# Optimization experiments

Hardware: AMD Instinct MI355X
Metric: run time of the kernel (lower is better)

The kernel has to match this reference:

```python
import jax, jax.numpy as jnp
import numpy as np

H = 16      # num_heads
D = 1024    # hidden_dim
HD = D // H # head_dim = 64


def setup_inputs() -> dict:
    key = jax.random.key(0)
    ks = jax.random.split(key, 9)
    s = 1.0 / np.sqrt(D)
    return {
        "hidden_states": jax.random.normal(ks[0], (2, 2048, D), dtype=jnp.float32),
        "wq": jax.random.uniform(ks[1], (D, D), jnp.float32, -s, s),
        "bq": jax.random.uniform(ks[2], (D,), jnp.float32, -s, s),
        "wk": jax.random.uniform(ks[3], (D, D), jnp.float32, -s, s),
        "bk": jax.random.uniform(ks[4], (D,), jnp.float32, -s, s),
        "wv": jax.random.uniform(ks[5], (D, D), jnp.float32, -s, s),
        "bv": jax.random.uniform(ks[6], (D,), jnp.float32, -s, s),
        "wo": jax.random.uniform(ks[7], (D, D), jnp.float32, -s, s),
        "bo": jax.random.uniform(ks[8], (D,), jnp.float32, -s, s),
    }


def reference(hidden_states, wq, bq, wk, bk, wv, bv, wo, bo):
    B, L, _ = hidden_states.shape
    scale = HD ** -0.5
    # projections: [B,L,D] -> [B,H,L,HD]
    def split_heads(x):
        return x.reshape(B, L, H, HD).transpose(0, 2, 1, 3)
    q = split_heads(hidden_states @ wq.T + bq)
    k = split_heads(hidden_states @ wk.T + bk)
    v = split_heads(hidden_states @ wv.T + bv)
    # explicit [B,H,L,L] scores + softmax + weighted sum (faithful to source)
    scores = jnp.einsum("bhqd,bhkd->bhqk", q, k) * scale
    attn = jax.nn.softmax(scores, axis=-1)
    out = jnp.einsum("bhqk,bhkd->bhqd", attn, v)
    out = out.transpose(0, 2, 1, 3).reshape(B, L, D)
    return out @ wo.T + bo
```

## Files before the change

kernel.cpp:

```cpp
#include <hip/hip_runtime.h>
#include <math.h>

#define BATCH  2
#define SEQ    2048
#define NH     16
#define DMODEL 1024
#define DHEAD  64

typedef short short8 __attribute__((ext_vector_type(8)));
typedef float f32x4 __attribute__((ext_vector_type(4)));

#define QSCALE 0.18033688011112042f

__device__ __forceinline__ ushort f2bf(float f) {
  unsigned int u = __builtin_bit_cast(unsigned int, f);
  u = (u + 0x7FFFu + ((u >> 16) & 1u)) >> 16;
  return (ushort)u;
}

__device__ __forceinline__ unsigned int cvtpk(float lo, float hi) {
  unsigned int r;
  asm("v_cvt_pk_bf16_f32 %0, %1, %2" : "=v"(r) : "v"(lo), "v"(hi));
  return r;
}

#define P32SWAP(a, b) \
  asm("v_permlane32_swap_b32 %0, %1" : "+v"(a), "+v"(b))
#define P16SWAP(a, b) \
  asm("v_permlane16_swap_b32 %0, %1" : "+v"(a), "+v"(b))

__global__ __launch_bounds__(256) void cast_all(
    const float* __restrict__ hs, const float* __restrict__ wq,
    const float* __restrict__ wk, const float* __restrict__ wv,
    const float* __restrict__ wo,
    ushort* __restrict__ hsb, ushort* __restrict__ wqb,
    ushort* __restrict__ wkb, ushort* __restrict__ wvb,
    ushort* __restrict__ wob) {
  const int z = blockIdx.y;
  const float* s = (z == 0) ? hs : (z == 1) ? wq : (z == 2) ? wk
                   : (z == 3) ? wv : wo;
  ushort* d = (z == 0) ? hsb : (z == 1) ? wqb : (z == 2) ? wkb
              : (z == 3) ? wvb : wob;
  const int n = (z == 0) ? BATCH * SEQ * DMODEL : DMODEL * DMODEL;
  const int i = (blockIdx.x * 256 + threadIdx.x) * 8;
  if (i < n) {
    const float4 a = *(const float4*)(s + i);
    const float4 b = *(const float4*)(s + i + 4);
    short8 o;
    o[0] = (short)f2bf(a.x); o[1] = (short)f2bf(a.y);
    o[2] = (short)f2bf(a.z); o[3] = (short)f2bf(a.w);
    o[4] = (short)f2bf(b.x); o[5] = (short)f2bf(b.y);
    o[6] = (short)f2bf(b.z); o[7] = (short)f2bf(b.w);
    *(short8*)(d + i) = o;
  }
}

__device__ __forceinline__ void mfma_gemm_core(
    const ushort* __restrict__ X, const ushort* __restrict__ W,
    f32x4 (&acc)[4][2]) {
  __shared__ ushort Al[128][40];
  __shared__ ushort Bl[128][40];
  const int tid = threadIdx.x;
  const int lane = tid & 63;
  const int w8 = tid >> 6;
  const int wm = w8 >> 2;
  const int wn = w8 & 3;
  const int m16 = lane & 15;
  const int g4 = lane >> 4;
  const int m0 = blockIdx.y << 7;
  const int n0 = blockIdx.x << 7;

  const int srow = tid >> 2;
  const int sseg = (tid & 3) << 3;
  const ushort* ap = X + (size_t)(m0 + srow) * DMODEL + sseg;
  const ushort* wp = W + (size_t)(n0 + srow) * DMODEL + sseg;

  short8 pa = *(const short8*)(ap);
  short8 pb = *(const short8*)(wp);

  for (int kt = 0; kt < DMODEL / 32; ++kt) {
    __syncthreads();
    *(short8*)&Al[srow][sseg] = pa;
    *(short8*)&Bl[srow][sseg] = pb;
    __syncthreads();
    if (kt < DMODEL / 32 - 1) {
      pa = *(const short8*)(ap + (kt + 1) * 32);
      pb = *(const short8*)(wp + (kt + 1) * 32);
    }
    short8 af[4], bf[2];
#pragma unroll
    for (int mi = 0; mi < 4; ++mi)
      af[mi] = *(const short8*)&Al[(wm << 6) + (mi << 4) + m16][g4 << 3];
#pragma unroll
    for (int ni = 0; ni < 2; ++ni)
      bf[ni] = *(const short8*)&Bl[(wn << 5) + (ni << 4) + m16][g4 << 3];
#pragma unroll
    for (int mi = 0; mi < 4; ++mi)
#pragma unroll
      for (int ni = 0; ni < 2; ++ni)
        acc[mi][ni] = __builtin_amdgcn_mfma_f32_16x16x32_bf16(
            af[mi], bf[ni], acc[mi][ni], 0, 0, 0);
  }
}

__global__ __launch_bounds__(512) void qkv_mfma(
    const ushort* __restrict__ X,
    const ushort* __restrict__ wqb, const ushort* __restrict__ wkb,
    const ushort* __restrict__ wvb,
    const float* __restrict__ bq, const float* __restrict__ bk,
    const float* __restrict__ bv,
    ushort* __restrict__ Qb, ushort* __restrict__ Kb,
    ushort* __restrict__ Vb) {
  const int z = blockIdx.z;
  const ushort* W = (z == 0) ? wqb : (z == 1) ? wkb : wvb;
  const float* bias = (z == 0) ? bq : (z == 1) ? bk : bv;
  ushort* Y = (z == 0) ? Qb : (z == 1) ? Kb : Vb;
  const float oscale = (z == 0) ? QSCALE : 1.0f;

  f32x4 acc[4][2];
#pragma unroll
  for (int mi = 0; mi < 4; ++mi)
#pragma unroll
    for (int ni = 0; ni < 2; ++ni) acc[mi][ni] = (f32x4){0.f, 0.f, 0.f, 0.f};
  mfma_gemm_core(X, W, acc);

  const int tid = threadIdx.x;
  const int lane = tid & 63;
  const int w8 = tid >> 6;
  const int wm = w8 >> 2, wn = w8 & 3;
  const int m16 = lane & 15, g4 = lane >> 4;
  const int m0 = blockIdx.y << 7, n0 = blockIdx.x << 7;
#pragma unroll
  for (int ni = 0; ni < 2; ++ni) {
    const int col = n0 + (wn << 5) + (ni << 4) + m16;
    const float bv4 = bias[col];
#pragma unroll
    for (int mi = 0; mi < 4; ++mi)
#pragma unroll
      for (int r = 0; r < 4; ++r) {
        const int row = m0 + (wm << 6) + (mi << 4) + (g4 << 2) + r;
        Y[(size_t)row * DMODEL + col] = f2bf((acc[mi][ni][r] + bv4) * oscale);
      }
  }
}

__global__ __launch_bounds__(512) void oproj_mfma(
    const ushort* __restrict__ X, const ushort* __restrict__ wob,
    const float* __restrict__ bo, float* __restrict__ Y) {
  f32x4 acc[4][2];
#pragma unroll
  for (int mi = 0; mi < 4; ++mi)
#pragma unroll
    for (int ni = 0; ni < 2; ++ni) acc[mi][ni] = (f32x4){0.f, 0.f, 0.f, 0.f};
  mfma_gemm_core(X, wob, acc);

  const int tid = threadIdx.x;
  const int lane = tid & 63;
  const int w8 = tid >> 6;
  const int wm = w8 >> 2, wn = w8 & 3;
  const int m16 = lane & 15, g4 = lane >> 4;
  const int m0 = blockIdx.y << 7, n0 = blockIdx.x << 7;
#pragma unroll
  for (int ni = 0; ni < 2; ++ni) {
    const int col = n0 + (wn << 5) + (ni << 4) + m16;
    const float bv4 = bo[col];
#pragma unroll
    for (int mi = 0; mi < 4; ++mi)
#pragma unroll
      for (int r = 0; r < 4; ++r) {
        const int row = m0 + (wm << 6) + (mi << 4) + (g4 << 2) + r;
        Y[(size_t)row * DMODEL + col] = acc[mi][ni][r] + bv4;
      }
  }
}

__global__ __launch_bounds__(512, 4) void attn_mfma(
    const ushort* __restrict__ Q, const ushort* __restrict__ K,
    const ushort* __restrict__ V, ushort* __restrict__ O) {
  __shared__ ushort Klds[2][64][72];
  __shared__ ushort Vlds[2][64][72];

  const int tid = threadIdx.x;
  const int lane = tid & 63;
  const int wv = tid >> 6;
  const int m16 = lane & 15;
  const int g4 = lane >> 4;
  const int b = blockIdx.z;
  const int h = blockIdx.y;
  const int q0 = (blockIdx.x << 7) + (wv << 4);

  const size_t base = ((size_t)b * SEQ) * DMODEL + h * DHEAD;

  short8 qf[2];
  {
    const ushort* qp = Q + base + (size_t)(q0 + m16) * DMODEL + (g4 << 3);
    qf[0] = *(const short8*)(qp);
    qf[1] = *(const short8*)(qp + 32);
  }

  f32x4 oacc[4];
#pragma unroll
  for (int dt = 0; dt < 4; ++dt) oacc[dt] = (f32x4){0.f, 0.f, 0.f, 0.f};
  float mrow = -1e30f;
  float lsum = 0.f;

  const int skey = tid >> 3;
  const int sseg = tid & 7;
  const ushort* kgp = K + base + (size_t)skey * DMODEL + (sseg << 3);
  const ushort* vgp = V + base + (size_t)skey * DMODEL + (sseg << 3);
  const int vswz_key = skey ^ (sseg << 3);

  short8 kvec = *(const short8*)(kgp);
  short8 vvec = *(const short8*)(vgp);

  int p = 0;
  for (int kt = 0; kt < SEQ / 64; ++kt) {
    *(short8*)&Klds[p][skey][sseg << 3] = kvec;
#pragma unroll
    for (int i = 0; i < 8; ++i)
      Vlds[p][(sseg << 3) + i][vswz_key] = ((const ushort*)&vvec)[i];
    __syncthreads();
    if (kt + 1 < SEQ / 64) {
      const size_t koff = (size_t)(kt + 1) * 64 * DMODEL;
      kvec = *(const short8*)(kgp + koff);
      vvec = *(const short8*)(vgp + koff);
    }

    f32x4 s[4];
#pragma unroll
    for (int kt2 = 0; kt2 < 4; ++kt2) s[kt2] = (f32x4){0.f, 0.f, 0.f, 0.f};
    __builtin_amdgcn_s_setprio(1);
#pragma unroll
    for (int ks = 0; ks < 2; ++ks) {
#pragma unroll
      for (int kt2 = 0; kt2 < 4; ++kt2) {
        const short8 kf =
            *(const short8*)&Klds[p][(kt2 << 4) + m16][(ks << 5) + (g4 << 3)];
        s[kt2] =
            __builtin_amdgcn_mfma_f32_16x16x32_bf16(kf, qf[ks], s[kt2], 0, 0, 0);
      }
    }
    __builtin_amdgcn_s_setprio(0);

    float t0 = fmaxf(fmaxf(s[0][0], s[0][1]), fmaxf(s[0][2], s[0][3]));
    float t1 = fmaxf(fmaxf(s[1][0], s[1][1]), fmaxf(s[1][2], s[1][3]));
    float t2 = fmaxf(fmaxf(s[2][0], s[2][1]), fmaxf(s[2][2], s[2][3]));
    float t3 = fmaxf(fmaxf(s[3][0], s[3][1]), fmaxf(s[3][2], s[3][3]));
    float tred = fmaxf(fmaxf(t0, t1), fmaxf(t2, t3));
    tred = fmaxf(tred, __shfl_xor(tred, 16));
    tred = fmaxf(tred, __shfl_xor(tred, 32));
    if (!__all(tred <= mrow + 8.0f)) {
      const float mnew = fmaxf(mrow, tred);
      const float corr = exp2f(mrow - mnew);
      lsum *= corr;
      const float cb0 = __shfl(corr, (g4 << 2) + 0);
      const float cb1 = __shfl(corr, (g4 << 2) + 1);
      const float cb2 = __shfl(corr, (g4 << 2) + 2);
      const float cb3 = __shfl(corr, (g4 << 2) + 3);
#pragma unroll
      for (int dt = 0; dt < 4; ++dt) {
        oacc[dt][0] *= cb0; oacc[dt][1] *= cb1;
        oacc[dt][2] *= cb2; oacc[dt][3] *= cb3;
      }
      mrow = mnew;
    }
    float ps = 0.f;
#pragma unroll
    for (int kt2 = 0; kt2 < 4; ++kt2)
#pragma unroll
      for (int r = 0; r < 4; ++r) {
        const float pv = exp2f(s[kt2][r] - mrow);
        s[kt2][r] = pv;
        ps += pv;
      }
    lsum += ps;

    unsigned int W0 = cvtpk(s[0][0], s[0][1]);
    unsigned int W1 = cvtpk(s[0][2], s[0][3]);
    unsigned int W2 = cvtpk(s[1][0], s[1][1]);
    unsigned int W3 = cvtpk(s[1][2], s[1][3]);
    unsigned int W4 = cvtpk(s[2][0], s[2][1]);
    unsigned int W5 = cvtpk(s[2][2], s[2][3]);
    unsigned int W6 = cvtpk(s[3][0], s[3][1]);
    unsigned int W7 = cvtpk(s[3][2], s[3][3]);
    P32SWAP(W0, W2);
    P32SWAP(W1, W3);
    P32SWAP(W4, W6);
    P32SWAP(W5, W7);
    P16SWAP(W0, W2);
    P16SWAP(W1, W3);
    P16SWAP(W4, W6);
    P16SWAP(W5, W7);
    union { unsigned int u[4]; short8 v; } u0, u1;
    u0.u[0] = W0; u0.u[1] = W1; u0.u[2] = W2; u0.u[3] = W3;
    u1.u[0] = W4; u1.u[1] = W5; u1.u[2] = W6; u1.u[3] = W7;

    __builtin_amdgcn_s_setprio(1);
#pragma unroll
    for (int dt = 0; dt < 4; ++dt) {
      const int d = (dt << 4) + m16;
      const int swz = (d >> 3) << 3;
      const short8 vf0 = *(const short8*)&Vlds[p][d][(g4 << 3) ^ swz];
      oacc[dt] = __builtin_amdgcn_mfma_f32_16x16x32_bf16(
          u0.v, vf0, oacc[dt], 0, 0, 0);
      const short8 vf1 = *(const short8*)&Vlds[p][d][(32 + (g4 << 3)) ^ swz];
      oacc[dt] = __builtin_amdgcn_mfma_f32_16x16x32_bf16(
          u1.v, vf1, oacc[dt], 0, 0, 0);
    }
    __builtin_amdgcn_s_setprio(0);
    p ^= 1;
  }

  lsum += __shfl_xor(lsum, 16);
  lsum += __shfl_xor(lsum, 32);
  const float inv = 1.0f / lsum;
  const float inv0 = __shfl(inv, (g4 << 2) + 0);
  const float inv1 = __shfl(inv, (g4 << 2) + 1);
  const float inv2 = __shfl(inv, (g4 << 2) + 2);
  const float inv3 = __shfl(inv, (g4 << 2) + 3);
  const float invr[4] = {inv0, inv1, inv2, inv3};
#pragma unroll
  for (int r = 0; r < 4; ++r) {
    const size_t row = (size_t)(q0 + (g4 << 2) + r);
    ushort* op = O + ((size_t)b * SEQ + row) * DMODEL + h * DHEAD + m16;
#pragma unroll
    for (int dt = 0; dt < 4; ++dt) op[dt << 4] = f2bf(oacc[dt][r] * invr[r]);
  }
}

extern "C" void kernel_launch(void* const* d_in, const int* in_sizes, int n_in,
                              void* d_out, int out_size, void* d_ws,
                              size_t ws_size, hipStream_t stream) {
  const float* hs = (const float*)d_in[0];
  const float* wq = (const float*)d_in[1];
  const float* bq = (const float*)d_in[2];
  const float* wk = (const float*)d_in[3];
  const float* bk = (const float*)d_in[4];
  const float* wv = (const float*)d_in[5];
  const float* bv = (const float*)d_in[6];
  const float* wo = (const float*)d_in[7];
  const float* bo = (const float*)d_in[8];
  float* out = (float*)d_out;

  const size_t elems = (size_t)BATCH * SEQ * DMODEL;
  const size_t welems = (size_t)DMODEL * DMODEL;
  ushort* hsb = (ushort*)d_ws;
  ushort* wqb = hsb + elems;
  ushort* wkb = wqb + welems;
  ushort* wvb = wkb + welems;
  ushort* wob = wvb + welems;
  ushort* Qb = wob + welems;
  ushort* Kb = Qb + elems;
  ushort* Vb = Kb + elems;
  ushort* Ab = Vb + elems;

  cast_all<<<dim3((int)(elems / (256 * 8)), 5, 1), 256, 0, stream>>>(
      hs, wq, wk, wv, wo, hsb, wqb, wkb, wvb, wob);
  qkv_mfma<<<dim3(DMODEL / 128, (BATCH * SEQ) / 128, 3), 512, 0, stream>>>(
      hsb, wqb, wkb, wvb, bq, bk, bv, Qb, Kb, Vb);
  attn_mfma<<<dim3(SEQ / 128, NH, BATCH), 512, 0, stream>>>(Qb, Kb, Vb, Ab);
  oproj_mfma<<<dim3(DMODEL / 128, (BATCH * SEQ) / 128, 1), 512, 0, stream>>>(
      Ab, wob, bo, out);
}
```

Measured before the change: 138.3 us.

## Split attention over key halves with a separate merge kernel

```diff
diff --git a/kernel.cpp b/kernel.cpp
--- a/kernel.cpp
+++ b/kernel.cpp
@@ -6,6 +6,7 @@
 #define NH     16
 #define DMODEL 1024
 #define DHEAD  64
+#define NSPLIT 2
 
 typedef short short8 __attribute__((ext_vector_type(8)));
 typedef float f32x4 __attribute__((ext_vector_type(4)));
@@ -16,6 +17,11 @@
   unsigned int u = __builtin_bit_cast(unsigned int, f);
   u = (u + 0x7FFFu + ((u >> 16) & 1u)) >> 16;
   return (ushort)u;
+}
+
+__device__ __forceinline__ float bf2f(ushort u) {
+  const unsigned int v = ((unsigned int)u) << 16;
+  return __builtin_bit_cast(float, v);
 }
 
 __device__ __forceinline__ unsigned int cvtpk(float lo, float hi) {
@@ -174,9 +180,10 @@
   }
 }
 
-__global__ __launch_bounds__(512, 4) void attn_mfma(
+__global__ __launch_bounds__(512, 8) void attn_mfma(
     const ushort* __restrict__ Q, const ushort* __restrict__ K,
-    const ushort* __restrict__ V, ushort* __restrict__ O) {
+    const ushort* __restrict__ V, ushort* __restrict__ Opart,
+    float2* __restrict__ ml) {
   __shared__ ushort Klds[2][64][72];
   __shared__ ushort Vlds[2][64][72];
 
@@ -185,11 +192,13 @@
   const int wv = tid >> 6;
   const int m16 = lane & 15;
   const int g4 = lane >> 4;
-  const int b = blockIdx.z;
+  const int b = blockIdx.z >> 1;
+  const int split = blockIdx.z & 1;
   const int h = blockIdx.y;
   const int q0 = (blockIdx.x << 7) + (wv << 4);
 
   const size_t base = ((size_t)b * SEQ) * DMODEL + h * DHEAD;
+  const size_t elems = (size_t)BATCH * SEQ * DMODEL;
 
   short8 qf[2];
   {
@@ -206,21 +215,23 @@
 
   const int skey = tid >> 3;
   const int sseg = tid & 7;
-  const ushort* kgp = K + base + (size_t)skey * DMODEL + (sseg << 3);
-  const ushort* vgp = V + base + (size_t)skey * DMODEL + (sseg << 3);
+  const ushort* kgp =
+      K + base + (size_t)(split * 1024 + skey) * DMODEL + (sseg << 3);
+  const ushort* vgp =
+      V + base + (size_t)(split * 1024 + skey) * DMODEL + (sseg << 3);
   const int vswz_key = skey ^ (sseg << 3);
 
   short8 kvec = *(const short8*)(kgp);
   short8 vvec = *(const short8*)(vgp);
 
   int p = 0;
-  for (int kt = 0; kt < SEQ / 64; ++kt) {
+  for (int kt = 0; kt < 1024 / 64; ++kt) {
     *(short8*)&Klds[p][skey][sseg << 3] = kvec;
 #pragma unroll
     for (int i = 0; i < 8; ++i)
       Vlds[p][(sseg << 3) + i][vswz_key] = ((const ushort*)&vvec)[i];
     __syncthreads();
-    if (kt + 1 < SEQ / 64) {
+    if (kt + 1 < 1024 / 64) {
       const size_t koff = (size_t)(kt + 1) * 64 * DMODEL;
       kvec = *(const short8*)(kgp + koff);
       vvec = *(const short8*)(vgp + koff);
@@ -313,19 +324,56 @@
 
   lsum += __shfl_xor(lsum, 16);
   lsum += __shfl_xor(lsum, 32);
+  if (lane < 16) {
+    ml[(((size_t)split * BATCH + b) * NH + h) * SEQ + q0 + lane] =
+        make_float2(mrow, lsum);
+  }
   const float inv = 1.0f / lsum;
   const float inv0 = __shfl(inv, (g4 << 2) + 0);
   const float inv1 = __shfl(inv, (g4 << 2) + 1);
   const float inv2 = __shfl(inv, (g4 << 2) + 2);
   const float inv3 = __shfl(inv, (g4 << 2) + 3);
   const float invr[4] = {inv0, inv1, inv2, inv3};
+  ushort* obase = Opart + (size_t)split * elems;
 #pragma unroll
   for (int r = 0; r < 4; ++r) {
     const size_t row = (size_t)(q0 + (g4 << 2) + r);
-    ushort* op = O + ((size_t)b * SEQ + row) * DMODEL + h * DHEAD + m16;
+    ushort* op = obase + ((size_t)b * SEQ + row) * DMODEL + h * DHEAD + m16;
 #pragma unroll
     for (int dt = 0; dt < 4; ++dt) op[dt << 4] = f2bf(oacc[dt][r] * invr[r]);
   }
+}
+
+__global__ __launch_bounds__(256) void attn_merge(
+    ushort* __restrict__ Opart, const float2* __restrict__ ml) {
+  const size_t elems = (size_t)BATCH * SEQ * DMODEL;
+  const size_t e0 = ((size_t)blockIdx.x * 256 + threadIdx.x) * 8;
+  if (e0 >= elems) return;
+  const int b = (int)(e0 / ((size_t)SEQ * DMODEL));
+  const size_t rem = e0 % ((size_t)SEQ * DMODEL);
+  const int s = (int)(rem / DMODEL);
+  const int d = (int)(rem % DMODEL);
+  const int h = d >> 6;
+
+  const float2 ml0 = ml[(((size_t)0 * BATCH + b) * NH + h) * SEQ + s];
+  const float2 ml1 = ml[(((size_t)1 * BATCH + b) * NH + h) * SEQ + s];
+  const float m = fmaxf(ml0.x, ml1.x);
+  const float a0 = ml0.y * exp2f(ml0.x - m);
+  const float a1 = ml1.y * exp2f(ml1.x - m);
+  const float inv = 1.0f / (a0 + a1);
+  const float w0 = a0 * inv;
+  const float w1 = a1 * inv;
+
+  const short8 o0 = *(const short8*)(Opart + e0);
+  const short8 o1 = *(const short8*)(Opart + elems + e0);
+  short8 o;
+#pragma unroll
+  for (int j = 0; j < 8; ++j) {
+    const float v =
+        w0 * bf2f((ushort)o0[j]) + w1 * bf2f((ushort)o1[j]);
+    o[j] = (short)f2bf(v);
+  }
+  *(short8*)(Opart + e0) = o;
 }
 
 extern "C" void kernel_launch(void* const* d_in, const int* in_sizes, int n_in,
@@ -352,13 +400,17 @@
   ushort* Qb = wob + welems;
   ushort* Kb = Qb + elems;
   ushort* Vb = Kb + elems;
-  ushort* Ab = Vb + elems;
+  ushort* Opart = Vb + elems;
+  float2* ml = (float2*)(Opart + NSPLIT * elems);
 
   cast_all<<<dim3((int)(elems / (256 * 8)), 5, 1), 256, 0, stream>>>(
       hs, wq, wk, wv, wo, hsb, wqb, wkb, wvb, wob);
   qkv_mfma<<<dim3(DMODEL / 128, (BATCH * SEQ) / 128, 3), 512, 0, stream>>>(
       hsb, wqb, wkb, wvb, bq, bk, bv, Qb, Kb, Vb);
-  attn_mfma<<<dim3(SEQ / 128, NH, BATCH), 512, 0, stream>>>(Qb, Kb, Vb, Ab);
+  attn_mfma<<<dim3(SEQ / 128, NH, BATCH * NSPLIT), 512, 0, stream>>>(
+      Qb, Kb, Vb, Opart, ml);
+  attn_merge<<<dim3((int)(elems / (256 * 8)), 1, 1), 256, 0, stream>>>(
+      Opart, ml);
   oproj_mfma<<<dim3(DMODEL / 128, (BATCH * SEQ) / 128, 1), 512, 0, stream>>>(
-      Ab, wob, bo, out);
-}
+      Opart, wob, bo, out);
+}
```

Measured after the change: 213.4 us. 54.3% more time.
